# Kernel tuning notes

Hardware: AMD Instinct MI355X
Metric: run time of the kernel (lower is better)

The kernel has to match this reference:

```python
import jax, jax.numpy as jnp
import numpy as np

N_NODES = 20000
N_EDGES = 640000
F = 64       # n_features
B = 20       # n_basis
LN_EPS = 1e-5

act = jax.nn.silu

def _lin_init(key, fan_in, fan_out):
    return jax.random.normal(key, (fan_in, fan_out), dtype=jnp.float32) / np.sqrt(fan_in)

def setup_inputs() -> dict:
    key = jax.random.key(0)
    ks = jax.random.split(key, 18)
    inp = {
        "atom_node": jax.random.normal(ks[0], (N_NODES, F), dtype=jnp.float32),
        "force_node": jax.random.normal(ks[1], (N_NODES, 3, F), dtype=jnp.float32),
        "dir_edge": jax.random.normal(ks[2], (N_EDGES, 3), dtype=jnp.float32),
        "dist_edge": jax.random.uniform(ks[3], (N_EDGES, B), dtype=jnp.float32),
        "edge_index": jax.random.randint(ks[4], (2, N_EDGES), 0, N_NODES, dtype=jnp.int64),
        # message_nodepart: Linear(F,F)+act+Linear(F,F)
        "W1": _lin_init(ks[5], F, F), "b1": jnp.zeros((F,), jnp.float32),
        "W2": _lin_init(ks[6], F, F), "b2": jnp.zeros((F,), jnp.float32),
        # message_edgepart: Linear(B,F,bias=False)
        "We": _lin_init(ks[7], B, F),
        # equiv_message1/2: Linear(F,F,nobias)+act+Linear(F,F,nobias)
        "Wq1a": _lin_init(ks[8], F, F), "Wq1b": _lin_init(ks[9], F, F),
        "Wq2a": _lin_init(ks[10], F, F), "Wq2b": _lin_init(ks[11], F, F),
        # equiv_update: Linear(F,F,nobias)
        "Wu": _lin_init(ks[12], F, F),
        # LayerNorm(F)
        "gamma": jnp.ones((F,), jnp.float32), "beta": jnp.zeros((F,), jnp.float32),
    }
    return inp

def reference(atom_node, force_node, dir_edge, dist_edge, edge_index,
              W1, b1, W2, b2, We, Wq1a, Wq1b, Wq2a, Wq2b, Wu, gamma, beta):
    src, dst = edge_index[0], edge_index[1]
    n = atom_node.shape[0]

    # node part of the message: MLP over nodes [N,F]
    mn = act(atom_node @ W1 + b1) @ W2 + b2
    # edge part: [E,F]
    me = dist_edge @ We
    # message: elementwise product of edge part and both endpoint node parts [E,F]
    message = me * mn[src] * mn[dst]

    # invariant update: scatter-add messages to source nodes
    inv_update1 = jax.ops.segment_sum(message, src, num_segments=n)
    atom_node = atom_node + inv_update1

    # equivariant messages [E,3,F]
    em1_inv = act(message @ Wq1a) @ Wq1b            # [E,F]
    em2_inv = act(message @ Wq2a) @ Wq2b            # [E,F]
    equiv_msg = (em1_inv[:, None, :] * dir_edge[:, :, None]
                 + em2_inv[:, None, :] * force_node[dst])  # [E,3,F]
    force_update = jax.ops.segment_sum(equiv_msg, src, num_segments=n)
    force_node = force_node + force_update

    # invariant contraction of vector features: sum over the 3-dim
    inv_update2 = jnp.sum(force_node * (force_node @ Wu), axis=1)  # [N,F]
    atom_node = atom_node + inv_update2

    # LayerNorm over feature dim
    mu = jnp.mean(atom_node, axis=-1, keepdims=True)
    var = jnp.var(atom_node, axis=-1, keepdims=True)
    atom_node = (atom_node - mu) * jax.lax.rsqrt(var + LN_EPS) * gamma + beta

    return (atom_node, force_node)
```

## Files before the change

kernel.cpp:

```cpp
#include <hip/hip_runtime.h>

#define N_NODES 20000
#define N_EDGES 640000
#define FDIM 64
#define NB 20
#define LN_EPS 1e-5f

typedef __attribute__((ext_vector_type(8))) short bf16x8;
typedef __attribute__((ext_vector_type(4))) float f32x4;

#define SEL_HI 0x07060302u
#define SEL_LO 0x05040100u
#define MFMA16 __builtin_amdgcn_mfma_f32_16x16x32_bf16

__device__ __forceinline__ float silu_f(float x) { return x / (1.0f + __expf(-x)); }

__device__ __forceinline__ float bcast_lane(float v, int lane) {
    return __int_as_float(__builtin_amdgcn_readlane(__float_as_int(v), lane));
}

__device__ __forceinline__ unsigned bf16_rn(float x) {
    unsigned u = __float_as_uint(x);
    return (u + 0x7FFFu + ((u >> 16) & 1u)) >> 16;
}

__device__ __forceinline__ unsigned pack_split(float x) {
    unsigned h = bf16_rn(x);
    unsigned lo = bf16_rn(x - __uint_as_float(h << 16));
    return (h << 16) | lo;
}

__device__ __forceinline__ void load_afrag(const unsigned* rowPtr, int kh, int q,
                                           bf16x8* ahi, bf16x8* alo) {
    const uint4 ra = *(const uint4*)(rowPtr + kh * 32 + q * 8);
    const uint4 rb = *(const uint4*)(rowPtr + kh * 32 + q * 8 + 4);
    union { unsigned u[4]; bf16x8 v; } H, L;
    H.u[0] = __builtin_amdgcn_perm(ra.y, ra.x, SEL_HI);
    H.u[1] = __builtin_amdgcn_perm(ra.w, ra.z, SEL_HI);
    H.u[2] = __builtin_amdgcn_perm(rb.y, rb.x, SEL_HI);
    H.u[3] = __builtin_amdgcn_perm(rb.w, rb.z, SEL_HI);
    L.u[0] = __builtin_amdgcn_perm(ra.y, ra.x, SEL_LO);
    L.u[1] = __builtin_amdgcn_perm(ra.w, ra.z, SEL_LO);
    L.u[2] = __builtin_amdgcn_perm(rb.y, rb.x, SEL_LO);
    L.u[3] = __builtin_amdgcn_perm(rb.w, rb.z, SEL_LO);
    *ahi = H.v;
    *alo = L.v;
}

__device__ __forceinline__ void mm3(const unsigned* Bhi, const unsigned* Blo,
                                    bf16x8 ahi, bf16x8 alo, f32x4* acc, int kh, int l) {
#pragma unroll
    for (int c = 0; c < 4; ++c) {
        bf16x8 bh = *(const bf16x8*)(Bhi + (kh * 4 + c) * 256 + l * 4);
        bf16x8 bl = *(const bf16x8*)(Blo + (kh * 4 + c) * 256 + l * 4);
        acc[c] = MFMA16(ahi, bh, acc[c], 0, 0, 0);
        acc[c] = MFMA16(ahi, bl, acc[c], 0, 0, 0);
        acc[c] = MFMA16(alo, bh, acc[c], 0, 0, 0);
    }
}

__global__ __launch_bounds__(256) void node_mlp_kernel(
    const float* __restrict__ atom, const float* __restrict__ W1, const float* __restrict__ b1,
    const float* __restrict__ W2, const float* __restrict__ b2, float* __restrict__ mn)
{
    __shared__ float W1s[FDIM][FDIM];
    __shared__ float W2s[FDIM][FDIM];
    const int f = threadIdx.x, ty = threadIdx.y;
    const int tid = ty * 64 + f;
    for (int i = tid; i < FDIM * FDIM; i += 256) {
        ((float*)W1s)[i] = W1[i];
        ((float*)W2s)[i] = W2[i];
    }
    __syncthreads();
    const float bb1 = b1[f], bb2 = b2[f];
    const int nw = gridDim.x * 4;
    for (int n = blockIdx.x * 4 + ty; n < N_NODES; n += nw) {
        const float a = atom[n * FDIM + f];
        float h = bb1;
        for (int g = 0; g < FDIM; ++g) h += bcast_lane(a, g) * W1s[g][f];
        h = silu_f(h);
        float o = bb2;
        for (int g = 0; g < FDIM; ++g) o += bcast_lane(h, g) * W2s[g][f];
        mn[n * FDIM + f] = o;
    }
}

__global__ __launch_bounds__(1024) void edge_kernel(
    const float* __restrict__ dist,
    const float* __restrict__ dir,
    const int* __restrict__ eidx,
    const float* __restrict__ mn,
    const float* __restrict__ We,
    const float* __restrict__ Wq1a, const float* __restrict__ Wq1b,
    const float* __restrict__ Wq2a, const float* __restrict__ Wq2b,
    const float* __restrict__ forceN,
    float* __restrict__ atomAcc,
    float* __restrict__ forceAcc)
{
    __shared__ __align__(16) unsigned Bfr[16384];
    __shared__ __align__(16) unsigned WeFr[2048];
    __shared__ __align__(16) unsigned Astg[16][16][76];

    const int l = threadIdx.x;
    const int ty = threadIdx.y;
    const int q = l >> 4, row = l & 15;

    for (int t = ty; t < 32; t += 16) {
        const int mm = t >> 3, kh = (t >> 2) & 1, c = t & 3;
        const float* W = (mm == 0) ? Wq1a : (mm == 1) ? Wq2a : (mm == 2) ? Wq1b : Wq2b;
        const int n = c * 16 + row;
        const int kb = kh * 32 + q * 8;
        unsigned* hiP = &Bfr[(((mm * 2 + 0) * 2 + kh) * 4 + c) * 256 + l * 4];
        unsigned* loP = &Bfr[(((mm * 2 + 1) * 2 + kh) * 4 + c) * 256 + l * 4];
#pragma unroll
        for (int i = 0; i < 4; ++i) {
            float w0 = W[(kb + 2 * i) * FDIM + n];
            float w1 = W[(kb + 2 * i + 1) * FDIM + n];
            unsigned h0 = bf16_rn(w0);
            unsigned l0 = bf16_rn(w0 - __uint_as_float(h0 << 16));
            unsigned h1 = bf16_rn(w1);
            unsigned l1 = bf16_rn(w1 - __uint_as_float(h1 << 16));
            hiP[i] = h0 | (h1 << 16);
            loP[i] = l0 | (l1 << 16);
        }
    }
    for (int c = ty; c < 4; c += 16) {
        const int n = c * 16 + row;
        unsigned* hiP = &WeFr[(0 * 4 + c) * 256 + l * 4];
        unsigned* loP = &WeFr[(1 * 4 + c) * 256 + l * 4];
#pragma unroll
        for (int i = 0; i < 4; ++i) {
            const int k0 = q * 8 + 2 * i, k1 = k0 + 1;
            float w0 = (k0 < NB) ? We[k0 * FDIM + n] : 0.0f;
            float w1 = (k1 < NB) ? We[k1 * FDIM + n] : 0.0f;
            unsigned h0 = bf16_rn(w0);
            unsigned l0 = bf16_rn(w0 - __uint_as_float(h0 << 16));
            unsigned h1 = bf16_rn(w1);
            unsigned l1 = bf16_rn(w1 - __uint_as_float(h1 << 16));
            hiP[i] = h0 | (h1 << 16);
            loP[i] = l0 | (l1 << 16);
        }
    }
    __syncthreads();

    const unsigned* B1aH = Bfr + 0 * 2048; const unsigned* B1aL = Bfr + 1 * 2048;
    const unsigned* B2aH = Bfr + 2 * 2048; const unsigned* B2aL = Bfr + 3 * 2048;
    const unsigned* B1bH = Bfr + 4 * 2048; const unsigned* B1bL = Bfr + 5 * 2048;
    const unsigned* B2bH = Bfr + 6 * 2048; const unsigned* B2bL = Bfr + 7 * 2048;
    const unsigned* WeH = WeFr;            const unsigned* WeL = WeFr + 1024;

    unsigned* stg = &Astg[ty][0][0];
    const unsigned* rowPtr = &Astg[ty][row][0];

    const int ngroups = N_EDGES / 16;
    const int stride = gridDim.x * 16;
    for (int grp = blockIdx.x * 16 + ty; grp < ngroups; grp += stride) {
        const int e0 = grp * 16;

        int ev = 0;
        if (l < 32) ev = eidx[(l < 16) ? (e0 + l) : (N_EDGES + e0 + (l - 16))];
        float dv = (l < 48) ? dir[e0 * 3 + l] : 0.0f;

        const float* dp = dist + (size_t)(e0 + row) * NB + q * 8;
        float4 da = {0.f, 0.f, 0.f, 0.f}, db = {0.f, 0.f, 0.f, 0.f};
        if (q < 2)       { da = *(const float4*)dp; db = *(const float4*)(dp + 4); }
        else if (q == 2) { da = *(const float4*)dp; }
        unsigned s0 = pack_split(da.x), s1 = pack_split(da.y);
        unsigned s2 = pack_split(da.z), s3 = pack_split(da.w);
        unsigned s4 = pack_split(db.x), s5 = pack_split(db.y);
        unsigned s6 = pack_split(db.z), s7 = pack_split(db.w);
        union { unsigned u[4]; bf16x8 v; } AH, AL;
        AH.u[0] = __builtin_amdgcn_perm(s1, s0, SEL_HI);
        AH.u[1] = __builtin_amdgcn_perm(s3, s2, SEL_HI);
        AH.u[2] = __builtin_amdgcn_perm(s5, s4, SEL_HI);
        AH.u[3] = __builtin_amdgcn_perm(s7, s6, SEL_HI);
        AL.u[0] = __builtin_amdgcn_perm(s1, s0, SEL_LO);
        AL.u[1] = __builtin_amdgcn_perm(s3, s2, SEL_LO);
        AL.u[2] = __builtin_amdgcn_perm(s5, s4, SEL_LO);
        AL.u[3] = __builtin_amdgcn_perm(s7, s6, SEL_LO);

        f32x4 me4[4];
#pragma unroll
        for (int c = 0; c < 4; ++c) me4[c] = (f32x4){0.f, 0.f, 0.f, 0.f};
        mm3(WeH, WeL, AH.v, AL.v, me4, 0, l);

#pragma unroll
        for (int c = 0; c < 4; ++c)
#pragma unroll
            for (int r = 0; r < 4; ++r)
                stg[(q * 4 + r) * 76 + (row + 16 * c)] = __float_as_uint(me4[c][r]);

#pragma unroll
        for (int j = 0; j < 16; ++j) {
            const int src = __builtin_amdgcn_readlane(ev, j);
            const int dst = __builtin_amdgcn_readlane(ev, 16 + j);
            const float me = __uint_as_float(stg[j * 76 + l]);
            const float m = me * mn[src * FDIM + l] * mn[dst * FDIM + l];
            atomicAdd(&atomAcc[src * FDIM + l], m);
            stg[j * 76 + l] = pack_split(m);
        }

        f32x4 acc1[4], acc2[4];
#pragma unroll
        for (int c = 0; c < 4; ++c) {
            acc1[c] = (f32x4){0.f, 0.f, 0.f, 0.f};
            acc2[c] = (f32x4){0.f, 0.f, 0.f, 0.f};
        }
#pragma unroll
        for (int kh = 0; kh < 2; ++kh) {
            bf16x8 ahi, alo;
            load_afrag(rowPtr, kh, q, &ahi, &alo);
            mm3(B1aH, B1aL, ahi, alo, acc1, kh, l);
            mm3(B2aH, B2aL, ahi, alo, acc2, kh, l);
        }
#pragma unroll
        for (int c = 0; c < 4; ++c)
#pragma unroll
            for (int r = 0; r < 4; ++r) {
                acc1[c][r] = silu_f(acc1[c][r]);
                acc2[c][r] = silu_f(acc2[c][r]);
            }

#pragma unroll
        for (int c = 0; c < 4; ++c)
#pragma unroll
            for (int r = 0; r < 4; ++r)
                stg[(q * 4 + r) * 76 + (row + 16 * c)] = pack_split(acc1[c][r]);

        f32x4 eacc1[4];
#pragma unroll
        for (int c = 0; c < 4; ++c) eacc1[c] = (f32x4){0.f, 0.f, 0.f, 0.f};
#pragma unroll
        for (int kh = 0; kh < 2; ++kh) {
            bf16x8 ahi, alo;
            load_afrag(rowPtr, kh, q, &ahi, &alo);
            mm3(B1bH, B1bL, ahi, alo, eacc1, kh, l);
        }

#pragma unroll
        for (int c = 0; c < 4; ++c)
#pragma unroll
            for (int r = 0; r < 4; ++r)
                stg[(q * 4 + r) * 76 + (row + 16 * c)] = pack_split(acc2[c][r]);

        f32x4 eacc2[4];
#pragma unroll
        for (int c = 0; c < 4; ++c) eacc2[c] = (f32x4){0.f, 0.f, 0.f, 0.f};
#pragma unroll
        for (int kh = 0; kh < 2; ++kh) {
            bf16x8 ahi, alo;
            load_afrag(rowPtr, kh, q, &ahi, &alo);
            mm3(B2bH, B2bL, ahi, alo, eacc2, kh, l);
        }

#pragma unroll
        for (int r = 0; r < 4; ++r) {
            const int eo = q * 4 + r;
            const int vs = __shfl(ev, eo);
            const int vd = __shfl(ev, 16 + eo);
            const float d0 = __shfl(dv, eo * 3 + 0);
            const float d1 = __shfl(dv, eo * 3 + 1);
            const float d2 = __shfl(dv, eo * 3 + 2);
            const float* fd = forceN + (size_t)vd * 3 * FDIM;
            float* fa = forceAcc + (size_t)vs * 3 * FDIM;
#pragma unroll
            for (int c = 0; c < 4; ++c) {
                const int n = row + 16 * c;
                const float a = eacc1[c][r];
                const float b = eacc2[c][r];
                atomicAdd(&fa[0 * FDIM + n], a * d0 + b * fd[0 * FDIM + n]);
                atomicAdd(&fa[1 * FDIM + n], a * d1 + b * fd[1 * FDIM + n]);
                atomicAdd(&fa[2 * FDIM + n], a * d2 + b * fd[2 * FDIM + n]);
            }
        }
    }
}

__global__ __launch_bounds__(256) void node_final_kernel(
    const float* __restrict__ Wu, const float* __restrict__ gamma, const float* __restrict__ beta,
    float* __restrict__ atomAcc,
    const float* __restrict__ forceOut)
{
    __shared__ float Wus[FDIM][FDIM];
    const int f = threadIdx.x, ty = threadIdx.y;
    const int tid = ty * 64 + f;
    for (int i = tid; i < FDIM * FDIM; i += 256) ((float*)Wus)[i] = Wu[i];
    __syncthreads();
    const float gg = gamma[f], bb = beta[f];
    const int nw = gridDim.x * 4;
    for (int n = blockIdx.x * 4 + ty; n < N_NODES; n += nw) {
        const float f0 = forceOut[((size_t)n * 3 + 0) * FDIM + f];
        const float f1 = forceOut[((size_t)n * 3 + 1) * FDIM + f];
        const float f2 = forceOut[((size_t)n * 3 + 2) * FDIM + f];
        float r0 = 0.0f, r1 = 0.0f, r2 = 0.0f;
#pragma unroll 8
        for (int g = 0; g < FDIM; ++g) {
            const float w = Wus[g][f];
            r0 += bcast_lane(f0, g) * w;
            r1 += bcast_lane(f1, g) * w;
            r2 += bcast_lane(f2, g) * w;
        }
        float a = atomAcc[n * FDIM + f] + (f0 * r0 + f1 * r1 + f2 * r2);
        float s = a;
#pragma unroll
        for (int off = 32; off >= 1; off >>= 1) s += __shfl_xor(s, off, 64);
        const float mu = s * (1.0f / 64.0f);
        const float d = a - mu;
        float v = d * d;
#pragma unroll
        for (int off = 32; off >= 1; off >>= 1) v += __shfl_xor(v, off, 64);
        v *= (1.0f / 64.0f);
        atomAcc[n * FDIM + f] = d * rsqrtf(v + LN_EPS) * gg + bb;
    }
}

extern "C" void kernel_launch(void* const* d_in, const int* in_sizes, int n_in,
                              void* d_out, int out_size, void* d_ws, size_t ws_size,
                              hipStream_t stream)
{
    const float* atom_node  = (const float*)d_in[0];
    const float* force_node = (const float*)d_in[1];
    const float* dir_edge   = (const float*)d_in[2];
    const float* dist_edge  = (const float*)d_in[3];
    const int*   edge_index = (const int*)d_in[4];
    const float* W1   = (const float*)d_in[5];
    const float* b1   = (const float*)d_in[6];
    const float* W2   = (const float*)d_in[7];
    const float* b2   = (const float*)d_in[8];
    const float* We   = (const float*)d_in[9];
    const float* Wq1a = (const float*)d_in[10];
    const float* Wq1b = (const float*)d_in[11];
    const float* Wq2a = (const float*)d_in[12];
    const float* Wq2b = (const float*)d_in[13];
    const float* Wu   = (const float*)d_in[14];
    const float* gamma = (const float*)d_in[15];
    const float* beta  = (const float*)d_in[16];

    float* atomOut  = (float*)d_out;
    float* forceOut = (float*)d_out + (size_t)N_NODES * FDIM;
    float* mn = (float*)d_ws;

    hipMemcpyAsync(atomOut, atom_node, (size_t)N_NODES * FDIM * sizeof(float),
                   hipMemcpyDeviceToDevice, stream);
    hipMemcpyAsync(forceOut, force_node, (size_t)N_NODES * 3 * FDIM * sizeof(float),
                   hipMemcpyDeviceToDevice, stream);

    dim3 blk4(64, 4);
    dim3 blk16(64, 16);
    node_mlp_kernel<<<512, blk4, 0, stream>>>(atom_node, W1, b1, W2, b2, mn);
    edge_kernel<<<256, blk16, 0, stream>>>(dist_edge, dir_edge, edge_index, mn, We,
                                           Wq1a, Wq1b, Wq2a, Wq2b, force_node,
                                           atomOut, forceOut);
    node_final_kernel<<<512, blk4, 0, stream>>>(Wu, gamma, beta, atomOut, forceOut);
}
```

Measured before the change: 606.8 us.

## Sort edges by source via counting sort and pre-reduce atomics per source run

Adds histogram, scan and permute kernels that bucket edges by source node and pack src, dst and direction into a meta array. The edge kernel then walks the sorted edges, summing invariant messages in registers across runs that share a source. When all 16 edges in a group share a source, it reduces the force contributions across lanes before issuing atomics. This is meant to cut atomic traffic and contention on the scatter-adds. In exchange it adds three kernels, a memset, extra workspace and gathered dist reads through the permutation, and it falls back to the old kernel when the workspace is too small.

```diff
diff --git a/kernel.cpp b/kernel.cpp
--- a/kernel.cpp
+++ b/kernel.cpp
@@ -85,10 +85,64 @@
     }
 }
 
-__global__ __launch_bounds__(1024) void edge_kernel(
+__global__ __launch_bounds__(256) void hist_kernel(const int* __restrict__ eidx, int* __restrict__ cursor) {
+    for (int e = blockIdx.x * 256 + threadIdx.x; e < N_EDGES; e += gridDim.x * 256)
+        atomicAdd(&cursor[eidx[e]], 1);
+}
+
+__global__ __launch_bounds__(1024) void scan_kernel(int* __restrict__ cursor) {
+    __shared__ int part[1024];
+    const int t = threadIdx.x;
+    int loc[20];
+    int s = 0;
+#pragma unroll
+    for (int i = 0; i < 20; ++i) {
+        const int idx = t * 20 + i;
+        const int v = (idx < N_NODES) ? cursor[idx] : 0;
+        loc[i] = s;
+        s += v;
+    }
+    part[t] = s;
+    __syncthreads();
+    for (int off = 1; off < 1024; off <<= 1) {
+        int v = (t >= off) ? part[t - off] : 0;
+        __syncthreads();
+        part[t] += v;
+        __syncthreads();
+    }
+    const int excl = (t == 0) ? 0 : part[t - 1];
+#pragma unroll
+    for (int i = 0; i < 20; ++i) {
+        const int idx = t * 20 + i;
+        if (idx < N_NODES) cursor[idx] = excl + loc[i];
+    }
+}
+
+__global__ __launch_bounds__(256) void permute_kernel(
+    const int* __restrict__ eidx, const float* __restrict__ dir,
+    int* __restrict__ cursor, int* __restrict__ perm, uint4* __restrict__ meta)
+{
+    for (int e = blockIdx.x * 256 + threadIdx.x; e < N_EDGES; e += gridDim.x * 256) {
+        const int src = eidx[e];
+        const int dst = eidx[N_EDGES + e];
+        const int pos = atomicAdd(&cursor[src], 1);
+        perm[pos] = e;
+        uint4 m0, m1;
+        m0.x = (unsigned)src;
+        m0.y = (unsigned)dst;
+        m0.z = __float_as_uint(dir[e * 3 + 0]);
+        m0.w = __float_as_uint(dir[e * 3 + 1]);
+        m1.x = __float_as_uint(dir[e * 3 + 2]);
+        m1.y = 0; m1.z = 0; m1.w = 0;
+        meta[(size_t)pos * 2] = m0;
+        meta[(size_t)pos * 2 + 1] = m1;
+    }
+}
+
+__global__ __launch_bounds__(1024) void edge_kernel_csr(
     const float* __restrict__ dist,
-    const float* __restrict__ dir,
-    const int* __restrict__ eidx,
+    const int* __restrict__ perm,
+    const uint2* __restrict__ meta,
     const float* __restrict__ mn,
     const float* __restrict__ We,
     const float* __restrict__ Wq1a, const float* __restrict__ Wq1b,
@@ -157,6 +211,242 @@
     for (int grp = blockIdx.x * 16 + ty; grp < ngroups; grp += stride) {
         const int e0 = grp * 16;
 
+        const uint2 md = meta[(size_t)e0 * 4 + l];
+        const float fx = __uint_as_float(md.x);
+        const float fy = __uint_as_float(md.y);
+
+        const int pe = perm[e0 + row];
+        const float* dp = dist + (size_t)pe * NB + q * 8;
+        float4 da = {0.f, 0.f, 0.f, 0.f}, db = {0.f, 0.f, 0.f, 0.f};
+        if (q < 2)       { da = *(const float4*)dp; db = *(const float4*)(dp + 4); }
+        else if (q == 2) { da = *(const float4*)dp; }
+        unsigned s0 = pack_split(da.x), s1 = pack_split(da.y);
+        unsigned s2 = pack_split(da.z), s3 = pack_split(da.w);
+        unsigned s4 = pack_split(db.x), s5 = pack_split(db.y);
+        unsigned s6 = pack_split(db.z), s7 = pack_split(db.w);
+        union { unsigned u[4]; bf16x8 v; } AH, AL;
+        AH.u[0] = __builtin_amdgcn_perm(s1, s0, SEL_HI);
+        AH.u[1] = __builtin_amdgcn_perm(s3, s2, SEL_HI);
+        AH.u[2] = __builtin_amdgcn_perm(s5, s4, SEL_HI);
+        AH.u[3] = __builtin_amdgcn_perm(s7, s6, SEL_HI);
+        AL.u[0] = __builtin_amdgcn_perm(s1, s0, SEL_LO);
+        AL.u[1] = __builtin_amdgcn_perm(s3, s2, SEL_LO);
+        AL.u[2] = __builtin_amdgcn_perm(s5, s4, SEL_LO);
+        AL.u[3] = __builtin_amdgcn_perm(s7, s6, SEL_LO);
+
+        f32x4 me4[4];
+#pragma unroll
+        for (int c = 0; c < 4; ++c) me4[c] = (f32x4){0.f, 0.f, 0.f, 0.f};
+        mm3(WeH, WeL, AH.v, AL.v, me4, 0, l);
+
+#pragma unroll
+        for (int c = 0; c < 4; ++c)
+#pragma unroll
+            for (int r = 0; r < 4; ++r)
+                stg[(q * 4 + r) * 76 + (row + 16 * c)] = __float_as_uint(me4[c][r]);
+
+        const int src0 = __builtin_amdgcn_readlane(md.x, 0);
+        int cur = src0;
+        float msum = 0.0f;
+        float mns = mn[(size_t)cur * FDIM + l];
+#pragma unroll
+        for (int j = 0; j < 16; ++j) {
+            const int sj = __builtin_amdgcn_readlane(md.x, 4 * j);
+            const int dj = __builtin_amdgcn_readlane(md.y, 4 * j);
+            if (sj != cur) {
+                atomicAdd(&atomAcc[(size_t)cur * FDIM + l], msum);
+                msum = 0.0f;
+                cur = sj;
+                mns = mn[(size_t)sj * FDIM + l];
+            }
+            const float me = __uint_as_float(stg[j * 76 + l]);
+            const float m = me * mns * mn[(size_t)dj * FDIM + l];
+            msum += m;
+            stg[j * 76 + l] = pack_split(m);
+        }
+        atomicAdd(&atomAcc[(size_t)cur * FDIM + l], msum);
+
+        f32x4 acc1[4], acc2[4];
+#pragma unroll
+        for (int c = 0; c < 4; ++c) {
+            acc1[c] = (f32x4){0.f, 0.f, 0.f, 0.f};
+            acc2[c] = (f32x4){0.f, 0.f, 0.f, 0.f};
+        }
+#pragma unroll
+        for (int kh = 0; kh < 2; ++kh) {
+            bf16x8 ahi, alo;
+            load_afrag(rowPtr, kh, q, &ahi, &alo);
+            mm3(B1aH, B1aL, ahi, alo, acc1, kh, l);
+            mm3(B2aH, B2aL, ahi, alo, acc2, kh, l);
+        }
+#pragma unroll
+        for (int c = 0; c < 4; ++c)
+#pragma unroll
+            for (int r = 0; r < 4; ++r) {
+                acc1[c][r] = silu_f(acc1[c][r]);
+                acc2[c][r] = silu_f(acc2[c][r]);
+            }
+
+#pragma unroll
+        for (int c = 0; c < 4; ++c)
+#pragma unroll
+            for (int r = 0; r < 4; ++r)
+                stg[(q * 4 + r) * 76 + (row + 16 * c)] = pack_split(acc1[c][r]);
+
+        f32x4 eacc1[4];
+#pragma unroll
+        for (int c = 0; c < 4; ++c) eacc1[c] = (f32x4){0.f, 0.f, 0.f, 0.f};
+#pragma unroll
+        for (int kh = 0; kh < 2; ++kh) {
+            bf16x8 ahi, alo;
+            load_afrag(rowPtr, kh, q, &ahi, &alo);
+            mm3(B1bH, B1bL, ahi, alo, eacc1, kh, l);
+        }
+
+#pragma unroll
+        for (int c = 0; c < 4; ++c)
+#pragma unroll
+            for (int r = 0; r < 4; ++r)
+                stg[(q * 4 + r) * 76 + (row + 16 * c)] = pack_split(acc2[c][r]);
+
+        f32x4 eacc2[4];
+#pragma unroll
+        for (int c = 0; c < 4; ++c) eacc2[c] = (f32x4){0.f, 0.f, 0.f, 0.f};
+#pragma unroll
+        for (int kh = 0; kh < 2; ++kh) {
+            bf16x8 ahi, alo;
+            load_afrag(rowPtr, kh, q, &ahi, &alo);
+            mm3(B2bH, B2bL, ahi, alo, eacc2, kh, l);
+        }
+
+        const int src15 = __builtin_amdgcn_readlane(md.x, 60);
+        if (src0 == src15) {
+            float t0[4] = {0.f, 0.f, 0.f, 0.f};
+            float t1[4] = {0.f, 0.f, 0.f, 0.f};
+            float t2[4] = {0.f, 0.f, 0.f, 0.f};
+#pragma unroll
+            for (int r = 0; r < 4; ++r) {
+                const int eo = q * 4 + r;
+                const int vd = __shfl((int)md.y, eo * 4);
+                const float d0 = __shfl(fx, eo * 4 + 1);
+                const float d1 = __shfl(fy, eo * 4 + 1);
+                const float d2 = __shfl(fx, eo * 4 + 2);
+                const float* fd = forceN + (size_t)vd * 3 * FDIM;
+#pragma unroll
+                for (int c = 0; c < 4; ++c) {
+                    const int n = row + 16 * c;
+                    const float a = eacc1[c][r];
+                    const float b = eacc2[c][r];
+                    t0[c] += a * d0 + b * fd[0 * FDIM + n];
+                    t1[c] += a * d1 + b * fd[1 * FDIM + n];
+                    t2[c] += a * d2 + b * fd[2 * FDIM + n];
+                }
+            }
+#pragma unroll
+            for (int c = 0; c < 4; ++c) {
+                t0[c] += __shfl_xor(t0[c], 16, 64); t0[c] += __shfl_xor(t0[c], 32, 64);
+                t1[c] += __shfl_xor(t1[c], 16, 64); t1[c] += __shfl_xor(t1[c], 32, 64);
+                t2[c] += __shfl_xor(t2[c], 16, 64); t2[c] += __shfl_xor(t2[c], 32, 64);
+            }
+            float* fa = forceAcc + (size_t)src0 * 3 * FDIM;
+#pragma unroll
+            for (int c = 0; c < 4; ++c) {
+                const float v = (q == 0) ? t0[c] : (q == 1) ? t1[c] : t2[c];
+                if (q < 3) atomicAdd(&fa[q * FDIM + row + 16 * c], v);
+            }
+        } else {
+#pragma unroll
+            for (int r = 0; r < 4; ++r) {
+                const int eo = q * 4 + r;
+                const int vs = __shfl((int)md.x, eo * 4);
+                const int vd = __shfl((int)md.y, eo * 4);
+                const float d0 = __shfl(fx, eo * 4 + 1);
+                const float d1 = __shfl(fy, eo * 4 + 1);
+                const float d2 = __shfl(fx, eo * 4 + 2);
+                const float* fd = forceN + (size_t)vd * 3 * FDIM;
+                float* fa = forceAcc + (size_t)vs * 3 * FDIM;
+#pragma unroll
+                for (int c = 0; c < 4; ++c) {
+                    const int n = row + 16 * c;
+                    const float a = eacc1[c][r];
+                    const float b = eacc2[c][r];
+                    atomicAdd(&fa[0 * FDIM + n], a * d0 + b * fd[0 * FDIM + n]);
+                    atomicAdd(&fa[1 * FDIM + n], a * d1 + b * fd[1 * FDIM + n]);
+                    atomicAdd(&fa[2 * FDIM + n], a * d2 + b * fd[2 * FDIM + n]);
+                }
+            }
+        }
+    }
+}
+
+__global__ __launch_bounds__(1024) void edge_kernel_old(
+    const float* __restrict__ dist, const float* __restrict__ dir,
+    const int* __restrict__ eidx, const float* __restrict__ mn,
+    const float* __restrict__ We,
+    const float* __restrict__ Wq1a, const float* __restrict__ Wq1b,
+    const float* __restrict__ Wq2a, const float* __restrict__ Wq2b,
+    const float* __restrict__ forceN,
+    float* __restrict__ atomAcc, float* __restrict__ forceAcc)
+{
+    __shared__ __align__(16) unsigned Bfr[16384];
+    __shared__ __align__(16) unsigned WeFr[2048];
+    __shared__ __align__(16) unsigned Astg[16][16][76];
+
+    const int l = threadIdx.x;
+    const int ty = threadIdx.y;
+    const int q = l >> 4, row = l & 15;
+
+    for (int t = ty; t < 32; t += 16) {
+        const int mm = t >> 3, kh = (t >> 2) & 1, c = t & 3;
+        const float* W = (mm == 0) ? Wq1a : (mm == 1) ? Wq2a : (mm == 2) ? Wq1b : Wq2b;
+        const int n = c * 16 + row;
+        const int kb = kh * 32 + q * 8;
+        unsigned* hiP = &Bfr[(((mm * 2 + 0) * 2 + kh) * 4 + c) * 256 + l * 4];
+        unsigned* loP = &Bfr[(((mm * 2 + 1) * 2 + kh) * 4 + c) * 256 + l * 4];
+#pragma unroll
+        for (int i = 0; i < 4; ++i) {
+            float w0 = W[(kb + 2 * i) * FDIM + n];
+            float w1 = W[(kb + 2 * i + 1) * FDIM + n];
+            unsigned h0 = bf16_rn(w0);
+            unsigned l0 = bf16_rn(w0 - __uint_as_float(h0 << 16));
+            unsigned h1 = bf16_rn(w1);
+            unsigned l1 = bf16_rn(w1 - __uint_as_float(h1 << 16));
+            hiP[i] = h0 | (h1 << 16);
+            loP[i] = l0 | (l1 << 16);
+        }
+    }
+    for (int c = ty; c < 4; c += 16) {
+        const int n = c * 16 + row;
+        unsigned* hiP = &WeFr[(0 * 4 + c) * 256 + l * 4];
+        unsigned* loP = &WeFr[(1 * 4 + c) * 256 + l * 4];
+#pragma unroll
+        for (int i = 0; i < 4; ++i) {
+            const int k0 = q * 8 + 2 * i, k1 = k0 + 1;
+            float w0 = (k0 < NB) ? We[k0 * FDIM + n] : 0.0f;
+            float w1 = (k1 < NB) ? We[k1 * FDIM + n] : 0.0f;
+            unsigned h0 = bf16_rn(w0);
+            unsigned l0 = bf16_rn(w0 - __uint_as_float(h0 << 16));
+            unsigned h1 = bf16_rn(w1);
+            unsigned l1 = bf16_rn(w1 - __uint_as_float(h1 << 16));
+            hiP[i] = h0 | (h1 << 16);
+            loP[i] = l0 | (l1 << 16);
+        }
+    }
+    __syncthreads();
+
+    const unsigned* B1aH = Bfr + 0 * 2048; const unsigned* B1aL = Bfr + 1 * 2048;
+    const unsigned* B2aH = Bfr + 2 * 2048; const unsigned* B2aL = Bfr + 3 * 2048;
+    const unsigned* B1bH = Bfr + 4 * 2048; const unsigned* B1bL = Bfr + 5 * 2048;
+    const unsigned* B2bH = Bfr + 6 * 2048; const unsigned* B2bL = Bfr + 7 * 2048;
+    const unsigned* WeH = WeFr;            const unsigned* WeL = WeFr + 1024;
+
+    unsigned* stg = &Astg[ty][0][0];
+    const unsigned* rowPtr = &Astg[ty][row][0];
+
+    const int ngroups = N_EDGES / 16;
+    const int stride = gridDim.x * 16;
+    for (int grp = blockIdx.x * 16 + ty; grp < ngroups; grp += stride) {
+        const int e0 = grp * 16;
         int ev = 0;
         if (l < 32) ev = eidx[(l < 16) ? (e0 + l) : (N_EDGES + e0 + (l - 16))];
         float dv = (l < 48) ? dir[e0 * 3 + l] : 0.0f;
@@ -183,7 +473,6 @@
 #pragma unroll
         for (int c = 0; c < 4; ++c) me4[c] = (f32x4){0.f, 0.f, 0.f, 0.f};
         mm3(WeH, WeL, AH.v, AL.v, me4, 0, l);
-
 #pragma unroll
         for (int c = 0; c < 4; ++c)
 #pragma unroll
@@ -220,13 +509,11 @@
                 acc1[c][r] = silu_f(acc1[c][r]);
                 acc2[c][r] = silu_f(acc2[c][r]);
             }
-
 #pragma unroll
         for (int c = 0; c < 4; ++c)
 #pragma unroll
             for (int r = 0; r < 4; ++r)
                 stg[(q * 4 + r) * 76 + (row + 16 * c)] = pack_split(acc1[c][r]);
-
         f32x4 eacc1[4];
 #pragma unroll
         for (int c = 0; c < 4; ++c) eacc1[c] = (f32x4){0.f, 0.f, 0.f, 0.f};
@@ -236,13 +523,11 @@
             load_afrag(rowPtr, kh, q, &ahi, &alo);
             mm3(B1bH, B1bL, ahi, alo, eacc1, kh, l);
         }
-
 #pragma unroll
         for (int c = 0; c < 4; ++c)
 #pragma unroll
             for (int r = 0; r < 4; ++r)
                 stg[(q * 4 + r) * 76 + (row + 16 * c)] = pack_split(acc2[c][r]);
-
         f32x4 eacc2[4];
 #pragma unroll
         for (int c = 0; c < 4; ++c) eacc2[c] = (f32x4){0.f, 0.f, 0.f, 0.f};
@@ -252,7 +537,6 @@
             load_afrag(rowPtr, kh, q, &ahi, &alo);
             mm3(B2bH, B2bL, ahi, alo, eacc2, kh, l);
         }
-
 #pragma unroll
         for (int r = 0; r < 4; ++r) {
             const int eo = q * 4 + r;
@@ -278,8 +562,7 @@
 
 __global__ __launch_bounds__(256) void node_final_kernel(
     const float* __restrict__ Wu, const float* __restrict__ gamma, const float* __restrict__ beta,
-    float* __restrict__ atomAcc,
-    const float* __restrict__ forceOut)
+    float* __restrict__ atomAcc, const float* __restrict__ forceOut)
 {
     __shared__ float Wus[FDIM][FDIM];
     const int f = threadIdx.x, ty = threadIdx.y;
@@ -338,7 +621,13 @@
 
     float* atomOut  = (float*)d_out;
     float* forceOut = (float*)d_out + (size_t)N_NODES * FDIM;
-    float* mn = (float*)d_ws;
+
+    char* ws = (char*)d_ws;
+    float* mn    = (float*)ws;
+    int* cursor  = (int*)(ws + 5120000);
+    int* perm    = (int*)(ws + 5200000);
+    uint4* meta  = (uint4*)(ws + 7760000);
+    const size_t NEED = 7760000 + (size_t)N_EDGES * 32;
 
     hipMemcpyAsync(atomOut, atom_node, (size_t)N_NODES * FDIM * sizeof(float),
                    hipMemcpyDeviceToDevice, stream);
@@ -348,8 +637,19 @@
     dim3 blk4(64, 4);
     dim3 blk16(64, 16);
     node_mlp_kernel<<<512, blk4, 0, stream>>>(atom_node, W1, b1, W2, b2, mn);
-    edge_kernel<<<256, blk16, 0, stream>>>(dist_edge, dir_edge, edge_index, mn, We,
-                                           Wq1a, Wq1b, Wq2a, Wq2b, force_node,
-                                           atomOut, forceOut);
+
+    if (ws_size >= NEED) {
+        hipMemsetAsync(cursor, 0, N_NODES * sizeof(int), stream);
+        hist_kernel<<<1024, 256, 0, stream>>>(edge_index, cursor);
+        scan_kernel<<<1, 1024, 0, stream>>>(cursor);
+        permute_kernel<<<1024, 256, 0, stream>>>(edge_index, dir_edge, cursor, perm, meta);
+        edge_kernel_csr<<<256, blk16, 0, stream>>>(dist_edge, perm, (const uint2*)meta, mn, We,
+                                                   Wq1a, Wq1b, Wq2a, Wq2b, force_node,
+                                                   atomOut, forceOut);
+    } else {
+        edge_kernel_old<<<256, blk16, 0, stream>>>(dist_edge, dir_edge, edge_index, mn, We,
+                                                   Wq1a, Wq1b, Wq2a, Wq2b, force_node,
+                                                   atomOut, forceOut);
+    }
     node_final_kernel<<<512, blk4, 0, stream>>>(Wu, gamma, beta, atomOut, forceOut);
 }
```

Measured after the change: 756.2 us. +24.6%, slower.

## Software-pipeline edge-group loads, prefetching next indices, distances and node messages

Applied to the files above, without the earlier changes.

Restructures the edge loop into a software pipeline. The next group's edge indices, directions and distance rows are loaded one iteration ahead, and the mn gathers for the next group are issued into registers during the current group's MFMA work. This is meant to hide global-memory latency of the random gathers behind compute. In exchange it raises register pressure (32 extra floats per lane plus prefetch buffers), which may reduce occupancy.

```diff
diff --git a/kernel.cpp b/kernel.cpp
--- a/kernel.cpp
+++ b/kernel.cpp
@@ -154,21 +154,38 @@
 
     const int ngroups = N_EDGES / 16;
     const int stride = gridDim.x * 16;
-    for (int grp = blockIdx.x * 16 + ty; grp < ngroups; grp += stride) {
-        const int e0 = grp * 16;
-
-        int ev = 0;
-        if (l < 32) ev = eidx[(l < 16) ? (e0 + l) : (N_EDGES + e0 + (l - 16))];
-        float dv = (l < 48) ? dir[e0 * 3 + l] : 0.0f;
-
+    int grp = blockIdx.x * 16 + ty;
+
+    int e0 = grp * 16;
+    int evA = (l < 32) ? eidx[(l < 16) ? (e0 + l) : (N_EDGES + e0 + (l - 16))] : 0;
+    float dvA = (l < 48) ? dir[e0 * 3 + l] : 0.0f;
+    float4 daA = {0.f, 0.f, 0.f, 0.f}, dbA = {0.f, 0.f, 0.f, 0.f};
+    {
         const float* dp = dist + (size_t)(e0 + row) * NB + q * 8;
-        float4 da = {0.f, 0.f, 0.f, 0.f}, db = {0.f, 0.f, 0.f, 0.f};
-        if (q < 2)       { da = *(const float4*)dp; db = *(const float4*)(dp + 4); }
-        else if (q == 2) { da = *(const float4*)dp; }
-        unsigned s0 = pack_split(da.x), s1 = pack_split(da.y);
-        unsigned s2 = pack_split(da.z), s3 = pack_split(da.w);
-        unsigned s4 = pack_split(db.x), s5 = pack_split(db.y);
-        unsigned s6 = pack_split(db.z), s7 = pack_split(db.w);
+        if (q < 2)       { daA = *(const float4*)dp; dbA = *(const float4*)(dp + 4); }
+        else if (q == 2) { daA = *(const float4*)dp; }
+    }
+    float mnS[16], mnD[16];
+#pragma unroll
+    for (int j = 0; j < 16; ++j) {
+        const int src = __builtin_amdgcn_readlane(evA, j);
+        const int dst = __builtin_amdgcn_readlane(evA, 16 + j);
+        mnS[j] = mn[(size_t)src * FDIM + l];
+        mnD[j] = mn[(size_t)dst * FDIM + l];
+    }
+
+    while (grp < ngroups) {
+        e0 = grp * 16;
+        const int grpN = grp + stride;
+        const int e0n = (grpN < ngroups) ? grpN * 16 : 0;
+
+        const int evB = (l < 32) ? eidx[(l < 16) ? (e0n + l) : (N_EDGES + e0n + (l - 16))] : 0;
+        const float dvB = (l < 48) ? dir[e0n * 3 + l] : 0.0f;
+
+        unsigned s0 = pack_split(daA.x), s1 = pack_split(daA.y);
+        unsigned s2 = pack_split(daA.z), s3 = pack_split(daA.w);
+        unsigned s4 = pack_split(dbA.x), s5 = pack_split(dbA.y);
+        unsigned s6 = pack_split(dbA.z), s7 = pack_split(dbA.w);
         union { unsigned u[4]; bf16x8 v; } AH, AL;
         AH.u[0] = __builtin_amdgcn_perm(s1, s0, SEL_HI);
         AH.u[1] = __builtin_amdgcn_perm(s3, s2, SEL_HI);
@@ -183,21 +200,34 @@
 #pragma unroll
         for (int c = 0; c < 4; ++c) me4[c] = (f32x4){0.f, 0.f, 0.f, 0.f};
         mm3(WeH, WeL, AH.v, AL.v, me4, 0, l);
-
 #pragma unroll
         for (int c = 0; c < 4; ++c)
 #pragma unroll
             for (int r = 0; r < 4; ++r)
                 stg[(q * 4 + r) * 76 + (row + 16 * c)] = __float_as_uint(me4[c][r]);
 
+        float4 daB = {0.f, 0.f, 0.f, 0.f}, dbB = {0.f, 0.f, 0.f, 0.f};
+        {
+            const float* dpn = dist + (size_t)(e0n + row) * NB + q * 8;
+            if (q < 2)       { daB = *(const float4*)dpn; dbB = *(const float4*)(dpn + 4); }
+            else if (q == 2) { daB = *(const float4*)dpn; }
+        }
+
 #pragma unroll
         for (int j = 0; j < 16; ++j) {
-            const int src = __builtin_amdgcn_readlane(ev, j);
-            const int dst = __builtin_amdgcn_readlane(ev, 16 + j);
+            const int src = __builtin_amdgcn_readlane(evA, j);
             const float me = __uint_as_float(stg[j * 76 + l]);
-            const float m = me * mn[src * FDIM + l] * mn[dst * FDIM + l];
-            atomicAdd(&atomAcc[src * FDIM + l], m);
+            const float m = me * mnS[j] * mnD[j];
+            atomicAdd(&atomAcc[(size_t)src * FDIM + l], m);
             stg[j * 76 + l] = pack_split(m);
+        }
+
+#pragma unroll
+        for (int j = 0; j < 16; ++j) {
+            const int srcN = __builtin_amdgcn_readlane(evB, j);
+            const int dstN = __builtin_amdgcn_readlane(evB, 16 + j);
+            mnS[j] = mn[(size_t)srcN * FDIM + l];
+            mnD[j] = mn[(size_t)dstN * FDIM + l];
         }
 
         f32x4 acc1[4], acc2[4];
@@ -226,7 +256,6 @@
 #pragma unroll
             for (int r = 0; r < 4; ++r)
                 stg[(q * 4 + r) * 76 + (row + 16 * c)] = pack_split(acc1[c][r]);
-
         f32x4 eacc1[4];
 #pragma unroll
         for (int c = 0; c < 4; ++c) eacc1[c] = (f32x4){0.f, 0.f, 0.f, 0.f};
@@ -242,7 +271,6 @@
 #pragma unroll
             for (int r = 0; r < 4; ++r)
                 stg[(q * 4 + r) * 76 + (row + 16 * c)] = pack_split(acc2[c][r]);
-
         f32x4 eacc2[4];
 #pragma unroll
         for (int c = 0; c < 4; ++c) eacc2[c] = (f32x4){0.f, 0.f, 0.f, 0.f};
@@ -256,11 +284,11 @@
 #pragma unroll
         for (int r = 0; r < 4; ++r) {
             const int eo = q * 4 + r;
-            const int vs = __shfl(ev, eo);
-            const int vd = __shfl(ev, 16 + eo);
-            const float d0 = __shfl(dv, eo * 3 + 0);
-            const float d1 = __shfl(dv, eo * 3 + 1);
-            const float d2 = __shfl(dv, eo * 3 + 2);
+            const int vs = __shfl(evA, eo);
+            const int vd = __shfl(evA, 16 + eo);
+            const float d0 = __shfl(dvA, eo * 3 + 0);
+            const float d1 = __shfl(dvA, eo * 3 + 1);
+            const float d2 = __shfl(dvA, eo * 3 + 2);
             const float* fd = forceN + (size_t)vd * 3 * FDIM;
             float* fa = forceAcc + (size_t)vs * 3 * FDIM;
 #pragma unroll
@@ -273,13 +301,18 @@
                 atomicAdd(&fa[2 * FDIM + n], a * d2 + b * fd[2 * FDIM + n]);
             }
         }
+
+        evA = evB;
+        dvA = dvB;
+        daA = daB;
+        dbA = dbB;
+        grp = grpN;
     }
 }
 
 __global__ __launch_bounds__(256) void node_final_kernel(
     const float* __restrict__ Wu, const float* __restrict__ gamma, const float* __restrict__ beta,
-    float* __restrict__ atomAcc,
-    const float* __restrict__ forceOut)
+    float* __restrict__ atomAcc, const float* __restrict__ forceOut)
 {
     __shared__ float Wus[FDIM][FDIM];
     const int f = threadIdx.x, ty = threadIdx.y;
```

New measurement: 595.1 us. No clear change (-1.9%).
